# Kernel optimization log

Measured on AMD Instinct MI355X. Metric: run time of the kernel, lower is better.

The kernel has to match this reference:

```python
import jax, jax.numpy as jnp
import numpy as np


def setup_inputs() -> dict:
    key = jax.random.key(0)
    ks = jax.random.split(key, 7)
    B, T, F, H = 512, 512, 64, 128
    s = 1.0 / np.sqrt(H)
    return {
        "x": jax.random.normal(ks[0], (B, T, F), dtype=jnp.float32),
        "W_ih": jax.random.uniform(ks[1], (3 * H, F), jnp.float32, -s, s),
        "W_hh": jax.random.uniform(ks[2], (3 * H, H), jnp.float32, -s, s),
        "b_ih": jax.random.uniform(ks[3], (3 * H,), jnp.float32, -s, s),
        "b_hh": jax.random.uniform(ks[4], (3 * H,), jnp.float32, -s, s),
        "W_out": jax.random.uniform(ks[5], (1, H), jnp.float32, -s, s),
        "b_out": jax.random.uniform(ks[6], (1,), jnp.float32, -s, s),
    }


def reference(x, W_ih, W_hh, b_ih, b_hh, W_out, b_out):
    B, T, F = x.shape
    H = W_hh.shape[1]
    # Precompute input projections for all timesteps: [T, B, 3H]
    x_t = jnp.transpose(x, (1, 0, 2))
    gi_all = jnp.einsum('tbf,gf->tbg', x_t, W_ih) + b_ih
    h0 = jnp.zeros((B, H), dtype=x.dtype)

    def step(h, gi):
        gh = h @ W_hh.T + b_hh  # [B, 3H]
        i_r, i_z, i_n = jnp.split(gi, 3, axis=-1)
        h_r, h_z, h_n = jnp.split(gh, 3, axis=-1)
        r = jax.nn.sigmoid(i_r + h_r)
        z = jax.nn.sigmoid(i_z + h_z)
        n = jnp.tanh(i_n + r * h_n)
        h_new = (1.0 - z) * n + z * h
        out = jnp.tanh(h_new @ W_out.T + b_out)[:, 0]  # [B]
        return h_new, out

    _, outs = jax.lax.scan(step, h0, gi_all)  # outs: [T, B]
    return outs.T  # [B, T]
```

## Files before the change

### kernel.cpp

```cpp
#include <hip/hip_runtime.h>
#include <math.h>

#define TSEQ 512
#define FDIM 64
#define HDIM 128
#define NB   512

#define SR 1.4426950408889634f
#define SN 2.8853900817779268f

typedef _Float16 f16x8 __attribute__((ext_vector_type(8)));
typedef _Float16 f16x4 __attribute__((ext_vector_type(4)));
typedef __fp16  fp16x2 __attribute__((ext_vector_type(2)));
typedef __attribute__((ext_vector_type(4))) float f32x4;

#define H_ROW 136
#define H_BUF (16 * H_ROW)
#define G_STEP ((size_t)96 * NB)

#if __has_builtin(__builtin_amdgcn_mfma_f32_16x16x16f16)
#define HAVE_MFMA16K16 1
__device__ __forceinline__ f32x4 mfma16k16(f16x4 a, f16x4 b, f32x4 c) {
    return __builtin_amdgcn_mfma_f32_16x16x16f16(a, b, c, 0, 0, 0);
}
#elif __has_builtin(__builtin_amdgcn_mfma_f32_16x16x16_f16)
#define HAVE_MFMA16K16 1
__device__ __forceinline__ f32x4 mfma16k16(f16x4 a, f16x4 b, f32x4 c) {
    return __builtin_amdgcn_mfma_f32_16x16x16_f16(a, b, c, 0, 0, 0);
}
#else
#define HAVE_MFMA16K16 0
#endif

__device__ __forceinline__ float exp2_hw(float x) {
#if __has_builtin(__builtin_amdgcn_exp2f)
    return __builtin_amdgcn_exp2f(x);
#else
    return exp2f(x);
#endif
}
__device__ __forceinline__ float fast_tanh(float x) {
    return 1.0f - 2.0f * __builtin_amdgcn_rcpf(1.0f + exp2_hw(SN * x));
}
__device__ __forceinline__ f32x4 mfma16f(f16x8 a, f16x8 b, f32x4 c) {
    return __builtin_amdgcn_mfma_f32_16x16x32_f16(a, b, c, 0, 0, 0);
}

union PU { fp16x2 h2[4]; f16x8 v; };
union GU { uint2 u; _Float16 h[4]; f16x4 v; };

__device__ __forceinline__ f16x8 pack_f16(float4 a, float4 b) {
    PU u;
    u.h2[0] = __builtin_amdgcn_cvt_pkrtz(a.x, a.y);
    u.h2[1] = __builtin_amdgcn_cvt_pkrtz(a.z, a.w);
    u.h2[2] = __builtin_amdgcn_cvt_pkrtz(b.x, b.y);
    u.h2[3] = __builtin_amdgcn_cvt_pkrtz(b.z, b.w);
    return u.v;
}

__device__ __forceinline__ void wg_barrier() {
    asm volatile("s_waitcnt lgkmcnt(0)" ::: "memory");
    __builtin_amdgcn_s_barrier();
    asm volatile("" ::: "memory");
}

__global__ __launch_bounds__(512)
void gi_gemm16(const float* __restrict__ x,
               const float* __restrict__ W_ih,
               const float* __restrict__ b_ih,
               const float* __restrict__ b_hh,
               uint2* __restrict__ gi)
{
    const int tid  = threadIdx.x;
    const int w    = tid >> 6;
    const int lane = tid & 63;
    const int g4   = lane >> 4;
    const int bcol = lane & 15;
    const int b0   = blockIdx.x * 16;
    const int t0   = blockIdx.y * 16;

    __shared__ __align__(16) _Float16 xt[16 * 1032 + 8];

    {
        const int bl = tid >> 5, q = tid & 31;
        const float* xp = x + ((size_t)(b0 + bl) * TSEQ + t0) * FDIM;
        _Float16* dst = &xt[bl * 1032];
        #pragma unroll
        for (int j = 0; j < 8; ++j) {
            float4 v = *(const float4*)(xp + j * 128 + q * 4);
            union { fp16x2 p[2]; uint2 u; } pu;
            pu.p[0] = __builtin_amdgcn_cvt_pkrtz(v.x, v.y);
            pu.p[1] = __builtin_amdgcn_cvt_pkrtz(v.z, v.w);
            *(uint2*)&dst[j * 128 + q * 4] = pu.u;
        }
    }

    f16x8 WihF[3][2];
    #pragma unroll
    for (int kd = 0; kd < 3; ++kd) {
        const float sc = (kd < 2) ? SR : SN;
        const int g = kd * 128 + w * 16 + bcol;
        #pragma unroll
        for (int kt = 0; kt < 2; ++kt) {
            const float* pw = W_ih + g * FDIM + kt * 32 + g4 * 8;
            f16x8 v;
            #pragma unroll
            for (int e = 0; e < 8; ++e) v[e] = (_Float16)(pw[e] * sc);
            WihF[kd][kt] = v;
        }
    }
    f32x4 biasR, biasZ, biasN;
    #pragma unroll
    for (int i = 0; i < 4; ++i) {
        const int gr = w * 16 + g4 * 4 + i;
        biasR[i] = (b_ih[gr]       + b_hh[gr])       * SR;
        biasZ[i] = (b_ih[128 + gr] + b_hh[128 + gr]) * SR;
        biasN[i] = b_ih[256 + gr] * SN;
    }
    __syncthreads();

    for (int tt = 0; tt < 16; ++tt) {
        const _Float16* xr = &xt[bcol * 1032 + tt * 64];
        f16x8 xf0 = *(const f16x8*)(xr + g4 * 8);
        f16x8 xf1 = *(const f16x8*)(xr + 32 + g4 * 8);

        f32x4 c0 = biasR, c1 = biasZ, c2 = biasN;
        c0 = mfma16f(WihF[0][0], xf0, c0);
        c0 = mfma16f(WihF[0][1], xf1, c0);
        c1 = mfma16f(WihF[1][0], xf0, c1);
        c1 = mfma16f(WihF[1][1], xf1, c1);
        c2 = mfma16f(WihF[2][0], xf0, c2);
        c2 = mfma16f(WihF[2][1], xf1, c2);

        GU g0, g1, g2;
        #pragma unroll
        for (int i = 0; i < 4; ++i) {
            g0.h[i] = (_Float16)c0[i];
            g1.h[i] = (_Float16)c1[i];
            g2.h[i] = (_Float16)c2[i];
        }
        const int t = t0 + tt;
        const size_t base = ((size_t)t * 96 + w * 4 + g4) * NB + (b0 + bcol);
        gi[base]           = g0.u;
        gi[base + 32 * NB] = g1.u;
        gi[base + 64 * NB] = g2.u;
    }
}

__global__ __launch_bounds__(512)
void out_final(const float* __restrict__ pp,
               const float* __restrict__ b_out,
               float* __restrict__ out)
{
    const int t = blockIdx.x;
    const int b = threadIdx.x;
    float acc = b_out[0];
    const float* p = pp + (size_t)t * 32 * NB + b;
    #pragma unroll
    for (int c = 0; c < 32; ++c) acc += p[(size_t)c * NB];
    out[(size_t)b * TSEQ + t] = fast_tanh(acc);
}

__global__ __launch_bounds__(512, 2)
void gru_rec(const float* __restrict__ W_hh,
             const float* __restrict__ b_hh,
             const float* __restrict__ W_out,
             const uint2* __restrict__ gi,
             float* __restrict__ pp)
{
    const int tid  = threadIdx.x;
    const int wid  = tid >> 6;
    const int lane = tid & 63;
    const int g4   = lane >> 4;
    const int bcol = lane & 15;
    const int b0   = blockIdx.x * 16;

    __shared__ __align__(16) _Float16 h_s[3][16][H_ROW];

    f16x4 iden;
    #pragma unroll
    for (int e = 0; e < 4; ++e)
        iden[e] = (bcol == g4 * 4 + e) ? (_Float16)1.0f : (_Float16)0.0f;
    const f32x4 zero4 = {0.f, 0.f, 0.f, 0.f};

    f16x8 WhhF[3][4];
    #pragma unroll
    for (int kd = 0; kd < 3; ++kd) {
        const float sc = (kd < 2) ? SR : SN;
        const int g = kd * 128 + wid * 16 + bcol;
        #pragma unroll
        for (int kt = 0; kt < 4; ++kt) {
            const float* pw = W_hh + g * HDIM + kt * 32 + g4 * 8;
            f16x8 v;
            #pragma unroll
            for (int e = 0; e < 8; ++e) v[e] = (_Float16)(pw[e] * sc);
            WhhF[kd][kt] = v;
        }
    }

    f32x4 biasNH;
    float wout_r[4], h_old[4];
    #pragma unroll
    for (int i = 0; i < 4; ++i) {
        const int gr = wid * 16 + g4 * 4 + i;
        biasNH[i] = b_hh[256 + gr] * SN;
        wout_r[i] = W_out[gr];
        h_old[i]  = 0.0f;
    }

    {
        unsigned* hp = (unsigned*)&h_s[0][0][0];
        for (int i = tid; i < H_BUF / 2; i += 512) hp[i] = 0u;
    }

    const uint2* gB = gi + ((size_t)wid * 4 + g4) * NB + (b0 + bcol);
    GU r0s, z0s, n0s, r1s, z1s, n1s, r2s, z2s, n2s, r3s, z3s, n3s;
    r0s.u = gB[0];              z0s.u = gB[32 * NB];          n0s.u = gB[64 * NB];
    r1s.u = gB[1*G_STEP];       z1s.u = gB[1*G_STEP + 32*NB]; n1s.u = gB[1*G_STEP + 64*NB];
    r2s.u = gB[2*G_STEP];       z2s.u = gB[2*G_STEP + 32*NB]; n2s.u = gB[2*G_STEP + 64*NB];
    r3s.u = gB[3*G_STEP];       z3s.u = gB[3*G_STEP + 32*NB]; n3s.u = gB[3*G_STEP + 64*NB];
    const uint2* gPr = gB + 4 * G_STEP;
    const uint2* gPz = gPr + 32 * NB;
    const uint2* gPn = gPr + 64 * NB;

    float* ppp = pp + ((size_t)wid * 4 + g4) * NB + (b0 + bcol);

    const _Float16* hrd = &h_s[0][bcol][0];
    _Float16*       hwr = &h_s[0][bcol][wid * 16 + g4 * 4];

    __syncthreads();

#if HAVE_MFMA16K16
#define INJ(S) mfma16k16(iden, S.v, zero4)
#else
#define INJ(S) (f32x4){(float)S.h[0], (float)S.h[1], (float)S.h[2], (float)S.h[3]}
#endif

#define STEP(RB, WB, SL, RF)                                                  \
{                                                                             \
    f16x8 bh0 = *(const f16x8*)(hrd + (RB) * H_BUF + 0 * 32 + g4 * 8);        \
    f16x8 bh1 = *(const f16x8*)(hrd + (RB) * H_BUF + 1 * 32 + g4 * 8);        \
    f16x8 bh2 = *(const f16x8*)(hrd + (RB) * H_BUF + 2 * 32 + g4 * 8);        \
    f16x8 bh3 = *(const f16x8*)(hrd + (RB) * H_BUF + 3 * 32 + g4 * 8);        \
    f32x4 a0 = INJ(r##SL##s);                                                 \
    f32x4 a1 = INJ(z##SL##s);                                                 \
    f32x4 a2 = INJ(n##SL##s);                                                 \
    if (RF) {                                                                 \
        r##SL##s.u = *gPr; z##SL##s.u = *gPz; n##SL##s.u = *gPn;              \
        gPr += G_STEP; gPz += G_STEP; gPn += G_STEP;                          \
    }                                                                         \
    f32x4 a3 = biasNH;                                                        \
    a0 = mfma16f(WhhF[0][0], bh0, a0);                                        \
    a1 = mfma16f(WhhF[1][0], bh0, a1);                                        \
    a3 = mfma16f(WhhF[2][0], bh0, a3);                                        \
    a0 = mfma16f(WhhF[0][1], bh1, a0);                                        \
    a1 = mfma16f(WhhF[1][1], bh1, a1);                                        \
    a3 = mfma16f(WhhF[2][1], bh1, a3);                                        \
    a0 = mfma16f(WhhF[0][2], bh2, a0);                                        \
    a1 = mfma16f(WhhF[1][2], bh2, a1);                                        \
    a3 = mfma16f(WhhF[2][2], bh2, a3);                                        \
    a0 = mfma16f(WhhF[0][3], bh3, a0);                                        \
    a1 = mfma16f(WhhF[1][3], bh3, a1);                                        \
    a3 = mfma16f(WhhF[2][3], bh3, a3);                                        \
    float psum = 0.0f;                                                        \
    float hn[4];                                                              \
    _Pragma("unroll")                                                         \
    for (int i = 0; i < 4; ++i) {                                             \
        float r = __builtin_amdgcn_rcpf(1.0f + exp2_hw(-a0[i]));              \
        float z = __builtin_amdgcn_rcpf(1.0f + exp2_hw(-a1[i]));              \
        float y = fmaf(r, a3[i], a2[i]);                                      \
        float n = fmaf(-2.0f, __builtin_amdgcn_rcpf(1.0f + exp2_hw(y)), 1.0f);\
        hn[i] = fmaf(z, h_old[i] - n, n);                                     \
        h_old[i] = hn[i];                                                     \
        psum = fmaf(wout_r[i], hn[i], psum);                                  \
    }                                                                         \
    {                                                                         \
        union { fp16x2 p[2]; uint2 u; } hu;                                   \
        hu.p[0] = __builtin_amdgcn_cvt_pkrtz(hn[0], hn[1]);                   \
        hu.p[1] = __builtin_amdgcn_cvt_pkrtz(hn[2], hn[3]);                   \
        *(uint2*)(hwr + (WB) * H_BUF) = hu.u;                                 \
    }                                                                         \
    *ppp = psum;                                                              \
    ppp += 32 * NB;                                                           \
    wg_barrier();                                                             \
}

    for (int tt = 0; tt < 42; ++tt) {
        STEP(0,1,0,1) STEP(1,2,1,1) STEP(2,0,2,1) STEP(0,1,3,1)
        STEP(1,2,0,1) STEP(2,0,1,1) STEP(0,1,2,1) STEP(1,2,3,1)
        STEP(2,0,0,1) STEP(0,1,1,1) STEP(1,2,2,1) STEP(2,0,3,1)
    }
    STEP(0,1,0,1) STEP(1,2,1,1) STEP(2,0,2,1) STEP(0,1,3,1)
    STEP(1,2,0,0) STEP(2,0,1,0) STEP(0,1,2,0) STEP(1,2,3,0)

#undef STEP
#undef INJ
}

__global__ __launch_bounds__(512, 2)
void gru_fb(const float* __restrict__ x,
            const float* __restrict__ W_ih,
            const float* __restrict__ W_hh,
            const float* __restrict__ b_ih,
            const float* __restrict__ b_hh,
            const float* __restrict__ W_out,
            const float* __restrict__ b_out,
            float* __restrict__ out)
{
    const int tid  = threadIdx.x;
    const int wid  = tid >> 6;
    const int lane = tid & 63;
    const int g4   = lane >> 4;
    const int bcol = lane & 15;
    const int b0   = blockIdx.x * 16;

    __shared__ __align__(16) _Float16 h_s[3][16][H_ROW];
    __shared__ __align__(16) float ps_s[3][16][12];

    f16x8 WhhF[3][4];
    f16x8 WihF[3][2];
    #pragma unroll
    for (int kd = 0; kd < 3; ++kd) {
        const float sc = (kd < 2) ? SR : SN;
        const int g = kd * 128 + wid * 16 + bcol;
        #pragma unroll
        for (int kt = 0; kt < 4; ++kt) {
            const float* pw = W_hh + g * HDIM + kt * 32 + g4 * 8;
            f16x8 v;
            #pragma unroll
            for (int e = 0; e < 8; ++e) v[e] = (_Float16)(pw[e] * sc);
            WhhF[kd][kt] = v;
        }
        #pragma unroll
        for (int kt = 0; kt < 2; ++kt) {
            const float* pw = W_ih + g * FDIM + kt * 32 + g4 * 8;
            f16x8 v;
            #pragma unroll
            for (int e = 0; e < 8; ++e) v[e] = (_Float16)(pw[e] * sc);
            WihF[kd][kt] = v;
        }
    }

    f32x4 biasR, biasZ, biasNI, biasNH;
    float wout_r[4], h_old[4];
    #pragma unroll
    for (int i = 0; i < 4; ++i) {
        const int gr = wid * 16 + g4 * 4 + i;
        biasR[i]  = (b_ih[gr]       + b_hh[gr])       * SR;
        biasZ[i]  = (b_ih[128 + gr] + b_hh[128 + gr]) * SR;
        biasNI[i] = b_ih[256 + gr] * SN;
        biasNH[i] = b_hh[256 + gr] * SN;
        wout_r[i] = W_out[gr];
        h_old[i]  = 0.0f;
    }
    const float bout = b_out[0];

    {
        unsigned* hp = (unsigned*)&h_s[0][0][0];
        for (int i = tid; i < H_BUF / 2; i += 512) hp[i] = 0u;
    }

    const float* xb = x + (size_t)(b0 + bcol) * TSEQ * FDIM;
    float4 sA0, sA1, sA2, sA3, sB0, sB1, sB2, sB3;
    sA0 = *(const float4*)(xb + g4 * 8);
    sA1 = *(const float4*)(xb + g4 * 8 + 4);
    sA2 = *(const float4*)(xb + 32 + g4 * 8);
    sA3 = *(const float4*)(xb + 32 + g4 * 8 + 4);
    {
        const float* xp1 = xb + FDIM;
        sB0 = *(const float4*)(xp1 + g4 * 8);
        sB1 = *(const float4*)(xp1 + g4 * 8 + 4);
        sB2 = *(const float4*)(xp1 + 32 + g4 * 8);
        sB3 = *(const float4*)(xp1 + 32 + g4 * 8 + 4);
    }
    f16x8 xf0 = pack_f16(sA0, sA1);
    f16x8 xf1 = pack_f16(sA2, sA3);

    __syncthreads();

    const bool outw = (wid == 0) && (lane < 16);
    float* outp = out + (size_t)(b0 + lane) * TSEQ;
    float o0 = 0.f, o1 = 0.f, o2 = 0.f, o3 = 0.f;
    int rb = 0, wb = 1;

    for (int t = 0; t < TSEQ; t += 4) {
        #pragma unroll
        for (int u = 0; u < 4; ++u) {
            const int s = t + u;

            if (outw && s > 0) {
                f32x4 q0 = *(const f32x4*)&ps_s[rb][lane][0];
                f32x4 q1 = *(const f32x4*)&ps_s[rb][lane][4];
                float sm = (q0[0] + q0[1]) + (q0[2] + q0[3])
                         + (q1[0] + q1[1]) + (q1[2] + q1[3]);
                float val = fast_tanh(sm + bout);
                if (u == 0) {
                    o3 = val;
                    *(float4*)(outp + (t - 4)) = make_float4(o0, o1, o2, o3);
                } else if (u == 1) o0 = val;
                else if (u == 2) o1 = val;
                else o2 = val;
            }

            {
                const int tl = (s + 2 < TSEQ) ? (s + 2) : (TSEQ - 1);
                const float* xp = xb + (size_t)tl * FDIM;
                if ((u & 1) == 0) {
                    sA0 = *(const float4*)(xp + g4 * 8);
                    sA1 = *(const float4*)(xp + g4 * 8 + 4);
                    sA2 = *(const float4*)(xp + 32 + g4 * 8);
                    sA3 = *(const float4*)(xp + 32 + g4 * 8 + 4);
                } else {
                    sB0 = *(const float4*)(xp + g4 * 8);
                    sB1 = *(const float4*)(xp + g4 * 8 + 4);
                    sB2 = *(const float4*)(xp + 32 + g4 * 8);
                    sB3 = *(const float4*)(xp + 32 + g4 * 8 + 4);
                }
            }
            f16x8 bh0 = *(const f16x8*)&h_s[rb][bcol][0 * 32 + g4 * 8];
            f16x8 bh1 = *(const f16x8*)&h_s[rb][bcol][1 * 32 + g4 * 8];
            f16x8 bh2 = *(const f16x8*)&h_s[rb][bcol][2 * 32 + g4 * 8];
            f16x8 bh3 = *(const f16x8*)&h_s[rb][bcol][3 * 32 + g4 * 8];

            f32x4 a0 = biasR, a1 = biasZ, a2 = biasNI, a3 = biasNH;
            a0 = mfma16f(WihF[0][0], xf0, a0);
            a0 = mfma16f(WihF[0][1], xf1, a0);
            a1 = mfma16f(WihF[1][0], xf0, a1);
            a1 = mfma16f(WihF[1][1], xf1, a1);
            a2 = mfma16f(WihF[2][0], xf0, a2);
            a2 = mfma16f(WihF[2][1], xf1, a2);

            a0 = mfma16f(WhhF[0][0], bh0, a0);
            a1 = mfma16f(WhhF[1][0], bh0, a1);
            a3 = mfma16f(WhhF[2][0], bh0, a3);
            a0 = mfma16f(WhhF[0][1], bh1, a0);
            a1 = mfma16f(WhhF[1][1], bh1, a1);
            a3 = mfma16f(WhhF[2][1], bh1, a3);
            a0 = mfma16f(WhhF[0][2], bh2, a0);
            a1 = mfma16f(WhhF[1][2], bh2, a1);
            a3 = mfma16f(WhhF[2][2], bh2, a3);
            a0 = mfma16f(WhhF[0][3], bh3, a0);
            a1 = mfma16f(WhhF[1][3], bh3, a1);
            a3 = mfma16f(WhhF[2][3], bh3, a3);

            float psum = 0.0f;
            _Float16 h16[4];
            #pragma unroll
            for (int i = 0; i < 4; ++i) {
                float r  = __builtin_amdgcn_rcpf(1.0f + exp2_hw(-a0[i]));
                float z  = __builtin_amdgcn_rcpf(1.0f + exp2_hw(-a1[i]));
                float y  = fmaf(r, a3[i], a2[i]);
                float n  = fmaf(-2.0f,
                                __builtin_amdgcn_rcpf(1.0f + exp2_hw(y)), 1.0f);
                float hn = fmaf(z, h_old[i] - n, n);
                h_old[i] = hn;
                h16[i]   = (_Float16)hn;
                psum = fmaf(wout_r[i], hn, psum);
            }

            union { _Float16 h[4]; uint2 u; } hu;
            hu.h[0] = h16[0]; hu.h[1] = h16[1];
            hu.h[2] = h16[2]; hu.h[3] = h16[3];
            *(uint2*)&h_s[wb][bcol][wid * 16 + g4 * 4] = hu.u;

            psum += __shfl_xor(psum, 16);
            psum += __shfl_xor(psum, 32);
            if (lane < 16) ps_s[wb][lane][wid] = psum;

            if ((u & 1) == 0) {
                xf0 = pack_f16(sB0, sB1);
                xf1 = pack_f16(sB2, sB3);
            } else {
                xf0 = pack_f16(sA0, sA1);
                xf1 = pack_f16(sA2, sA3);
            }

            wg_barrier();
            rb = wb; wb = (wb == 2) ? 0 : wb + 1;
        }
    }

    if (outw) {
        f32x4 q0 = *(const f32x4*)&ps_s[2][lane][0];
        f32x4 q1 = *(const f32x4*)&ps_s[2][lane][4];
        float sm = (q0[0] + q0[1]) + (q0[2] + q0[3])
                 + (q1[0] + q1[1]) + (q1[2] + q1[3]);
        o3 = fast_tanh(sm + bout);
        *(float4*)(outp + (TSEQ - 4)) = make_float4(o0, o1, o2, o3);
    }
}

extern "C" void kernel_launch(void* const* d_in, const int* in_sizes, int n_in,
                              void* d_out, int out_size, void* d_ws, size_t ws_size,
                              hipStream_t stream) {
    const float* x     = (const float*)d_in[0];
    const float* W_ih  = (const float*)d_in[1];
    const float* W_hh  = (const float*)d_in[2];
    const float* b_ih  = (const float*)d_in[3];
    const float* b_hh  = (const float*)d_in[4];
    const float* W_out = (const float*)d_in[5];
    const float* b_out = (const float*)d_in[6];
    float* out = (float*)d_out;

    const size_t gi_bytes = (size_t)TSEQ * NB * 384 * sizeof(_Float16);
    const size_t pp_bytes = (size_t)TSEQ * 32 * NB * sizeof(float);

    if (ws_size >= gi_bytes + pp_bytes) {
        uint2* gi = (uint2*)d_ws;
        float* pp = (float*)((char*)d_ws + gi_bytes);
        gi_gemm16<<<dim3(32, 32), 512, 0, stream>>>(x, W_ih, b_ih, b_hh, gi);
        gru_rec<<<32, 512, 0, stream>>>(W_hh, b_hh, W_out, gi, pp);
        out_final<<<TSEQ, NB, 0, stream>>>(pp, b_out, out);
    } else {
        gru_fb<<<32, 512, 0, stream>>>(x, W_ih, W_hh, b_ih, b_hh,
                                       W_out, b_out, out);
    }
}
```

Before: 341.3 us.

## Fuse input-projection GEMM and GRU recurrence into producer/consumer persistent kernel

Merges the separate input-projection GEMM kernel and the recurrent kernel into one launch. Producer blocks compute gi chunks in time order and bump per-time-tile atomic counters, while 32 consumer blocks run the recurrence and spin-wait on those counters before reading each tile. This overlaps the projection with the serial recurrence and removes a kernel boundary. It relies on all blocks being co-resident to avoid deadlock and adds a memset plus polling overhead.

After: 644.9 us. 1.89x slower.

```diff
diff --git a/kernel.cpp b/kernel.cpp
--- a/kernel.cpp
+++ b/kernel.cpp
@@ -17,6 +17,10 @@
 #define H_ROW 136
 #define H_BUF (16 * H_ROW)
 #define G_STEP ((size_t)96 * NB)
+
+#define CONS_BLOCKS 32
+#define PROD_BLOCKS 224
+#define NCHUNK 1024
 
 #if __has_builtin(__builtin_amdgcn_mfma_f32_16x16x16f16)
 #define HAVE_MFMA16K16 1
@@ -62,89 +66,6 @@
     asm volatile("s_waitcnt lgkmcnt(0)" ::: "memory");
     __builtin_amdgcn_s_barrier();
     asm volatile("" ::: "memory");
-}
-
-__global__ __launch_bounds__(512)
-void gi_gemm16(const float* __restrict__ x,
-               const float* __restrict__ W_ih,
-               const float* __restrict__ b_ih,
-               const float* __restrict__ b_hh,
-               uint2* __restrict__ gi)
-{
-    const int tid  = threadIdx.x;
-    const int w    = tid >> 6;
-    const int lane = tid & 63;
-    const int g4   = lane >> 4;
-    const int bcol = lane & 15;
-    const int b0   = blockIdx.x * 16;
-    const int t0   = blockIdx.y * 16;
-
-    __shared__ __align__(16) _Float16 xt[16 * 1032 + 8];
-
-    {
-        const int bl = tid >> 5, q = tid & 31;
-        const float* xp = x + ((size_t)(b0 + bl) * TSEQ + t0) * FDIM;
-        _Float16* dst = &xt[bl * 1032];
-        #pragma unroll
-        for (int j = 0; j < 8; ++j) {
-            float4 v = *(const float4*)(xp + j * 128 + q * 4);
-            union { fp16x2 p[2]; uint2 u; } pu;
-            pu.p[0] = __builtin_amdgcn_cvt_pkrtz(v.x, v.y);
-            pu.p[1] = __builtin_amdgcn_cvt_pkrtz(v.z, v.w);
-            *(uint2*)&dst[j * 128 + q * 4] = pu.u;
-        }
-    }
-
-    f16x8 WihF[3][2];
-    #pragma unroll
-    for (int kd = 0; kd < 3; ++kd) {
-        const float sc = (kd < 2) ? SR : SN;
-        const int g = kd * 128 + w * 16 + bcol;
-        #pragma unroll
-        for (int kt = 0; kt < 2; ++kt) {
-            const float* pw = W_ih + g * FDIM + kt * 32 + g4 * 8;
-            f16x8 v;
-            #pragma unroll
-            for (int e = 0; e < 8; ++e) v[e] = (_Float16)(pw[e] * sc);
-            WihF[kd][kt] = v;
-        }
-    }
-    f32x4 biasR, biasZ, biasN;
-    #pragma unroll
-    for (int i = 0; i < 4; ++i) {
-        const int gr = w * 16 + g4 * 4 + i;
-        biasR[i] = (b_ih[gr]       + b_hh[gr])       * SR;
-        biasZ[i] = (b_ih[128 + gr] + b_hh[128 + gr]) * SR;
-        biasN[i] = b_ih[256 + gr] * SN;
-    }
-    __syncthreads();
-
-    for (int tt = 0; tt < 16; ++tt) {
-        const _Float16* xr = &xt[bcol * 1032 + tt * 64];
-        f16x8 xf0 = *(const f16x8*)(xr + g4 * 8);
-        f16x8 xf1 = *(const f16x8*)(xr + 32 + g4 * 8);
-
-        f32x4 c0 = biasR, c1 = biasZ, c2 = biasN;
-        c0 = mfma16f(WihF[0][0], xf0, c0);
-        c0 = mfma16f(WihF[0][1], xf1, c0);
-        c1 = mfma16f(WihF[1][0], xf0, c1);
-        c1 = mfma16f(WihF[1][1], xf1, c1);
-        c2 = mfma16f(WihF[2][0], xf0, c2);
-        c2 = mfma16f(WihF[2][1], xf1, c2);
-
-        GU g0, g1, g2;
-        #pragma unroll
-        for (int i = 0; i < 4; ++i) {
-            g0.h[i] = (_Float16)c0[i];
-            g1.h[i] = (_Float16)c1[i];
-            g2.h[i] = (_Float16)c2[i];
-        }
-        const int t = t0 + tt;
-        const size_t base = ((size_t)t * 96 + w * 4 + g4) * NB + (b0 + bcol);
-        gi[base]           = g0.u;
-        gi[base + 32 * NB] = g1.u;
-        gi[base + 64 * NB] = g2.u;
-    }
 }
 
 __global__ __launch_bounds__(512)
@@ -162,20 +83,107 @@
 }
 
 __global__ __launch_bounds__(512, 2)
-void gru_rec(const float* __restrict__ W_hh,
-             const float* __restrict__ b_hh,
-             const float* __restrict__ W_out,
-             const uint2* __restrict__ gi,
-             float* __restrict__ pp)
+void gru_fused(const float* __restrict__ x,
+               const float* __restrict__ W_ih,
+               const float* __restrict__ W_hh,
+               const float* __restrict__ b_ih,
+               const float* __restrict__ b_hh,
+               const float* __restrict__ W_out,
+               uint2* __restrict__ gi,
+               float* __restrict__ pp,
+               int* __restrict__ cnt)
 {
+    __shared__ __align__(16) unsigned char smem[16 * 1032 * 2 + 32];
+
     const int tid  = threadIdx.x;
     const int wid  = tid >> 6;
     const int lane = tid & 63;
     const int g4   = lane >> 4;
     const int bcol = lane & 15;
-    const int b0   = blockIdx.x * 16;
-
-    __shared__ __align__(16) _Float16 h_s[3][16][H_ROW];
+
+    if (blockIdx.x >= CONS_BLOCKS) {
+        _Float16* xt = (_Float16*)smem;
+        const int pid = blockIdx.x - CONS_BLOCKS;
+        const int w = wid;
+
+        f16x8 WihF[3][2];
+        #pragma unroll
+        for (int kd = 0; kd < 3; ++kd) {
+            const float sc = (kd < 2) ? SR : SN;
+            const int g = kd * 128 + w * 16 + bcol;
+            #pragma unroll
+            for (int kt = 0; kt < 2; ++kt) {
+                const float* pw = W_ih + g * FDIM + kt * 32 + g4 * 8;
+                f16x8 v;
+                #pragma unroll
+                for (int e = 0; e < 8; ++e) v[e] = (_Float16)(pw[e] * sc);
+                WihF[kd][kt] = v;
+            }
+        }
+        f32x4 biasR, biasZ, biasN;
+        #pragma unroll
+        for (int i = 0; i < 4; ++i) {
+            const int gr = w * 16 + g4 * 4 + i;
+            biasR[i] = (b_ih[gr]       + b_hh[gr])       * SR;
+            biasZ[i] = (b_ih[128 + gr] + b_hh[128 + gr]) * SR;
+            biasN[i] = b_ih[256 + gr] * SN;
+        }
+
+        for (int c = pid; c < NCHUNK; c += PROD_BLOCKS) {
+            const int tau = c >> 5, bt = c & 31;
+            const int b0p = bt * 16, t0 = tau * 16;
+
+            __syncthreads();
+            {
+                const int bl = tid >> 5, q = tid & 31;
+                const float* xp = x + ((size_t)(b0p + bl) * TSEQ + t0) * FDIM;
+                _Float16* dst = &xt[bl * 1032];
+                #pragma unroll
+                for (int j = 0; j < 8; ++j) {
+                    float4 v = *(const float4*)(xp + j * 128 + q * 4);
+                    union { fp16x2 p[2]; uint2 u; } pu;
+                    pu.p[0] = __builtin_amdgcn_cvt_pkrtz(v.x, v.y);
+                    pu.p[1] = __builtin_amdgcn_cvt_pkrtz(v.z, v.w);
+                    *(uint2*)&dst[j * 128 + q * 4] = pu.u;
+                }
+            }
+            __syncthreads();
+
+            for (int tt = 0; tt < 16; ++tt) {
+                const _Float16* xr = &xt[bcol * 1032 + tt * 64];
+                f16x8 xf0 = *(const f16x8*)(xr + g4 * 8);
+                f16x8 xf1 = *(const f16x8*)(xr + 32 + g4 * 8);
+
+                f32x4 c0 = biasR, c1 = biasZ, c2 = biasN;
+                c0 = mfma16f(WihF[0][0], xf0, c0);
+                c0 = mfma16f(WihF[0][1], xf1, c0);
+                c1 = mfma16f(WihF[1][0], xf0, c1);
+                c1 = mfma16f(WihF[1][1], xf1, c1);
+                c2 = mfma16f(WihF[2][0], xf0, c2);
+                c2 = mfma16f(WihF[2][1], xf1, c2);
+
+                GU g0, g1, g2;
+                #pragma unroll
+                for (int i = 0; i < 4; ++i) {
+                    g0.h[i] = (_Float16)c0[i];
+                    g1.h[i] = (_Float16)c1[i];
+                    g2.h[i] = (_Float16)c2[i];
+                }
+                const int t = t0 + tt;
+                const size_t base = ((size_t)t * 96 + w * 4 + g4) * NB + (b0p + bcol);
+                gi[base]           = g0.u;
+                gi[base + 32 * NB] = g1.u;
+                gi[base + 64 * NB] = g2.u;
+            }
+            __threadfence();
+            __syncthreads();
+            if (tid == 0) atomicAdd(&cnt[tau], 1);
+        }
+        return;
+    }
+
+    _Float16* h_s = (_Float16*)smem;
+    const int b0 = blockIdx.x * 16;
 
     f16x4 iden;
     #pragma unroll
@@ -209,9 +217,23 @@
     }
 
     {
-        unsigned* hp = (unsigned*)&h_s[0][0][0];
+        unsigned* hp = (unsigned*)h_s;
         for (int i = tid; i < H_BUF / 2; i += 512) hp[i] = 0u;
     }
+
+    int done_tile = 0;
+#define WAIT_TILES(NEED)                                                      \
+    {                                                                         \
+        int nd_ = (NEED); if (nd_ > 31) nd_ = 31;                             \
+        while (done_tile <= nd_) {                                            \
+            while (__hip_atomic_load(&cnt[done_tile], __ATOMIC_ACQUIRE,       \
+                                     __HIP_MEMORY_SCOPE_AGENT) < 32)          \
+                __builtin_amdgcn_s_sleep(8);                                  \
+            ++done_tile;                                                      \
+        }                                                                     \
+    }
+
+    WAIT_TILES(0)
 
     const uint2* gB = gi + ((size_t)wid * 4 + g4) * NB + (b0 + bcol);
     GU r0s, z0s, n0s, r1s, z1s, n1s, r2s, z2s, n2s, r3s, z3s, n3s;
@@ -225,8 +247,8 @@
 
     float* ppp = pp + ((size_t)wid * 4 + g4) * NB + (b0 + bcol);
 
-    const _Float16* hrd = &h_s[0][bcol][0];
-    _Float16*       hwr = &h_s[0][bcol][wid * 16 + g4 * 4];
+    const _Float16* hrd = h_s + bcol * H_ROW;
+    _Float16*       hwr = h_s + bcol * H_ROW + wid * 16 + g4 * 4;
 
     __syncthreads();
 
@@ -286,15 +308,18 @@
 }
 
     for (int tt = 0; tt < 42; ++tt) {
+        WAIT_TILES((tt * 12 + 19) >> 4)
         STEP(0,1,0,1) STEP(1,2,1,1) STEP(2,0,2,1) STEP(0,1,3,1)
         STEP(1,2,0,1) STEP(2,0,1,1) STEP(0,1,2,1) STEP(1,2,3,1)
         STEP(2,0,0,1) STEP(0,1,1,1) STEP(1,2,2,1) STEP(2,0,3,1)
     }
+    WAIT_TILES(31)
     STEP(0,1,0,1) STEP(1,2,1,1) STEP(2,0,2,1) STEP(0,1,3,1)
     STEP(1,2,0,0) STEP(2,0,1,0) STEP(0,1,2,0) STEP(1,2,3,0)
 
 #undef STEP
 #undef INJ
+#undef WAIT_TILES
 }
 
 __global__ __launch_bounds__(512, 2)
@@ -502,14 +527,17 @@
     const float* b_out = (const float*)d_in[6];
     float* out = (float*)d_out;
 
-    const size_t gi_bytes = (size_t)TSEQ * NB * 384 * sizeof(_Float16);
-    const size_t pp_bytes = (size_t)TSEQ * 32 * NB * sizeof(float);
-
-    if (ws_size >= gi_bytes + pp_bytes) {
+    const size_t gi_bytes  = (size_t)TSEQ * NB * 384 * sizeof(_Float16);
+    const size_t pp_bytes  = (size_t)TSEQ * 32 * NB * sizeof(float);
+    const size_t cnt_bytes = 4096;
+
+    if (ws_size >= gi_bytes + pp_bytes + cnt_bytes) {
         uint2* gi = (uint2*)d_ws;
         float* pp = (float*)((char*)d_ws + gi_bytes);
-        gi_gemm16<<<dim3(32, 32), 512, 0, stream>>>(x, W_ih, b_ih, b_hh, gi);
-        gru_rec<<<32, 512, 0, stream>>>(W_hh, b_hh, W_out, gi, pp);
+        int*   cnt = (int*)((char*)d_ws + gi_bytes + pp_bytes);
+        hipMemsetAsync(cnt, 0, cnt_bytes, stream);
+        gru_fused<<<CONS_BLOCKS + PROD_BLOCKS, 512, 0, stream>>>(
+            x, W_ih, W_hh, b_ih, b_hh, W_out, gi, pp, cnt);
         out_final<<<TSEQ, NB, 0, stream>>>(pp, b_out, out);
     } else {
         gru_fb<<<32, 512, 0, stream>>>(x, W_ih, W_hh, b_ih, b_hh,
```
